# Performance work log

Measured on AMD Instinct MI355X. Metric: run time of the kernel, lower is better.

## Reference

```python
import jax, jax.numpy as jnp
import numpy as np

V = 16384  # points per mesh


def _nn_idx(q, r):
    """1-NN index into r for each row of q. q: [Vq,3], r: [Vr,3] -> [Vq] int32.

    Squared euclidean distance via ||q||^2 - 2 q.r + ||r||^2 (K=1 knn_points).
    """
    d = (jnp.sum(q * q, axis=-1, keepdims=True)
         - 2.0 * (q @ r.T)
         + jnp.sum(r * r, axis=-1)[None, :])  # [Vq, Vr]
    return jnp.argmin(d, axis=1)


def setup_inputs() -> dict:
    key = jax.random.key(0)
    k1, k2, k3, k4 = jax.random.split(key, 4)
    return {
        "pred_vertices": jax.random.normal(k1, (1, V, 3), dtype=jnp.float32),
        "trg_vertices": jax.random.normal(k2, (1, V, 3), dtype=jnp.float32),
        "pred_e": jax.random.normal(k3, (1, V, 3), dtype=jnp.float32),
        "trg_e": jax.random.normal(k4, (1, V, 3), dtype=jnp.float32),
    }


def reference(pred_vertices, trg_vertices, pred_e, trg_e):
    pv = pred_vertices[0]  # [V,3]
    tv = trg_vertices[0]   # [V,3]
    # knn_points runs under torch.no_grad() -> indices are constants
    trg2pred_idx = jax.lax.stop_gradient(_nn_idx(tv, pv))  # [V]
    pred2trg_idx = jax.lax.stop_gradient(_nn_idx(pv, tv))  # [V]
    loss_trg2pred = jnp.mean((trg_e - pred_e[:, trg2pred_idx, :]) ** 2)
    loss_pred2trg = jnp.mean((pred_e - trg_e[:, pred2trg_idx, :]) ** 2)
    return loss_trg2pred + loss_pred2trg
```

## Files before the change

### kernel.cpp

```cpp
#include <hip/hip_runtime.h>
#include <hip/hip_bf16.h>

#define NV 16384
#define NT 256
#define NTILES 512
#define RT_CHUNK 64
#define NCHUNK (NTILES / RT_CHUNK)
#define STG 32
#define QT_PER_BLOCK 8
#define NN_BX (NTILES / QT_PER_BLOCK)
#define RES_QPW 4
#define RES_QPB (4 * RES_QPW)
#define RES_BLOCKS (NV / RES_QPB)
#define NPART (2 * RES_BLOCKS)

typedef __attribute__((ext_vector_type(8))) short bf16x8;
typedef __attribute__((ext_vector_type(16))) float f32x16;

__device__ __forceinline__ short bf16bits(float f) {
    __hip_bfloat16 h = __float2bfloat16(f);
    return *reinterpret_cast<short*>(&h);
}
__device__ __forceinline__ float bf16tof(short s) {
    __hip_bfloat16 h = *reinterpret_cast<__hip_bfloat16*>(&s);
    return __bfloat162float(h);
}
__device__ __forceinline__ unsigned sortable(float f) {
    unsigned u = __float_as_uint(f);
    return (u & 0x80000000u) ? ~u : (u | 0x80000000u);
}
__device__ __forceinline__ float min3f(float a, float b, float c) {
    float r;
    asm("v_min3_f32 %0, %1, %2, %3" : "=v"(r) : "v"(a), "v"(b), "v"(c));
    return r;
}
__device__ __forceinline__ float tree16(const f32x16& c) {
    float t0 = min3f(c[0], c[1], c[2]);
    float t1 = min3f(c[3], c[4], c[5]);
    float t2 = min3f(c[6], c[7], c[8]);
    float t3 = min3f(c[9], c[10], c[11]);
    float t4 = min3f(c[12], c[13], c[14]);
    float s0 = min3f(t0, t1, c[15]);
    float s1 = min3f(t2, t3, t4);
    return fminf(s0, s1);
}

__device__ __forceinline__ bf16x8 make_a(float x, float y, float z, int half) {
    short hx = bf16bits(x), hy = bf16bits(y), hz = bf16bits(z);
    short lx = bf16bits(x - bf16tof(hx));
    short ly = bf16bits(y - bf16tof(hy));
    short lz = bf16bits(z - bf16tof(hz));
    float n  = 0.5f * fmaf(z, z, fmaf(y, y, x * x));
    short nh = bf16bits(n);
    short nl = bf16bits(n - bf16tof(nh));
    bf16x8 v;
    v[0] = half ? hz : hx;  v[1] = half ? nh : hy;
    v[2] = half ? nl : hz;  v[3] = half ? (short)0 : lx;
    v[4] = half ? (short)0 : ly;  v[5] = half ? (short)0 : lz;
    v[6] = half ? (short)0 : hx;  v[7] = half ? (short)0 : hy;
    return v;
}
__device__ __forceinline__ bf16x8 make_b(float x, float y, float z, int half) {
    short hx = bf16bits(x), hy = bf16bits(y), hz = bf16bits(z);
    short nhx = bf16bits(-x), nhy = bf16bits(-y), nhz = bf16bits(-z);
    short nlx = bf16bits(bf16tof(hx) - x);
    short nly = bf16bits(bf16tof(hy) - y);
    short nlz = bf16bits(bf16tof(hz) - z);
    const short one = 0x3F80;
    bf16x8 v;
    v[0] = half ? nlz : nhx;  v[1] = half ? one : nhy;
    v[2] = half ? one : nhz;  v[3] = half ? (short)0 : nhx;
    v[4] = half ? (short)0 : nhy;  v[5] = half ? (short)0 : nhz;
    v[6] = half ? (short)0 : nlx;  v[7] = half ? (short)0 : nly;
    return v;
}

__global__ __launch_bounds__(NT) void prep_kernel(
    const float* __restrict__ pred_v, const float* __restrict__ trg_v,
    short* __restrict__ Apack)
{
    int gid = blockIdx.x * NT + threadIdx.x;
    int d   = gid >> 15;
    int rem = gid & 32767;
    int t   = rem >> 6;
    int l   = rem & 63;
    const float* rpts = d ? trg_v : pred_v;
    int p = t * 32 + (l & 31);
    bf16x8 v = make_a(rpts[3 * p + 0], rpts[3 * p + 1], rpts[3 * p + 2], l >> 5);
    *(bf16x8*)(Apack + ((size_t)gid) * 8) = v;
}

__global__ __launch_bounds__(NT, 4) void nn_mfma_kernel(
    const float* __restrict__ pred_v, const float* __restrict__ trg_v,
    const short* __restrict__ Apack, unsigned long long* __restrict__ results)
{
    __shared__ short lds[STG * 512];
    const int tid = threadIdx.x, lane = tid & 63, w = tid >> 6;
    const int dir = blockIdx.z;
    const float* qpts = dir ? pred_v : trg_v;
    const int qt0 = blockIdx.x * QT_PER_BLOCK + w * 2;
    const int rtb = blockIdx.y * RT_CHUNK;
    const int half = lane >> 5;
    const size_t dbase = (size_t)dir * NTILES * 512;

    const int qp0 = qt0 * 32 + (lane & 31);
    bf16x8 b0 = make_b(qpts[3 * qp0 + 0], qpts[3 * qp0 + 1], qpts[3 * qp0 + 2], half);
    bf16x8 b1 = make_b(qpts[3 * (qp0 + 32) + 0], qpts[3 * (qp0 + 32) + 1],
                       qpts[3 * (qp0 + 32) + 2], half);

    float dmin0 = 1e30f, dmin1 = 1e30f;
    int bp0 = 0, bp1 = 0;
    const f32x16 zc = {};

    for (int g = 0; g < RT_CHUNK / STG; g++) {
        __syncthreads();
        const bf16x8* src = (const bf16x8*)(Apack + dbase + (size_t)(rtb + g * STG) * 512);
#pragma unroll
        for (int s = 0; s < (STG * 64) / NT; s++) {
            int slot = s * NT + tid;
            *(bf16x8*)(&lds[slot * 8]) = src[slot];
        }
        __syncthreads();
#pragma unroll 2
        for (int p = 0; p < STG / 2; p++) {
            bf16x8 a0 = *(const bf16x8*)(&lds[(2 * p) * 512 + lane * 8]);
            f32x16 c0 = __builtin_amdgcn_mfma_f32_32x32x16_bf16(a0, b0, zc, 0, 0, 0);
            f32x16 c1 = __builtin_amdgcn_mfma_f32_32x32x16_bf16(a0, b1, zc, 0, 0, 0);
            float u0 = tree16(c0), u1 = tree16(c1);
            bf16x8 a1 = *(const bf16x8*)(&lds[(2 * p + 1) * 512 + lane * 8]);
            f32x16 d0 = __builtin_amdgcn_mfma_f32_32x32x16_bf16(a1, b0, zc, 0, 0, 0);
            f32x16 d1 = __builtin_amdgcn_mfma_f32_32x32x16_bf16(a1, b1, zc, 0, 0, 0);
            float m0 = fminf(u0, tree16(d0));
            float m1 = fminf(u1, tree16(d1));
            int pid = blockIdx.y * (RT_CHUNK / 2) + g * (STG / 2) + p;
            bool lt0 = m0 < dmin0; dmin0 = lt0 ? m0 : dmin0; bp0 = lt0 ? pid : bp0;
            bool lt1 = m1 < dmin1; dmin1 = lt1 ? m1 : dmin1; bp1 = lt1 ? pid : bp1;
        }
    }

    unsigned long long k0 = ((unsigned long long)sortable(dmin0) << 32) | (unsigned)bp0;
    unsigned long long k1 = ((unsigned long long)sortable(dmin1) << 32) | (unsigned)bp1;
    unsigned long long o0 = __shfl_xor(k0, 32); k0 = (o0 < k0) ? o0 : k0;
    unsigned long long o1 = __shfl_xor(k1, 32); k1 = (o1 < k1) ? o1 : k1;
    if (lane < 32) {
        size_t base = ((size_t)dir * NCHUNK + blockIdx.y) * NV;
        results[base + qt0 * 32 + lane] = k0;
        results[base + (qt0 + 1) * 32 + lane] = k1;
    }
}

__global__ __launch_bounds__(NT) void resolve_loss_kernel(
    const float* __restrict__ pred_v, const float* __restrict__ trg_v,
    const float* __restrict__ pred_e, const float* __restrict__ trg_e,
    const unsigned long long* __restrict__ results, float* __restrict__ partials)
{
    const int dir = blockIdx.y;
    const float* qpts = dir ? pred_v : trg_v;
    const float* rpts = dir ? trg_v : pred_v;
    const float* qe_b = dir ? pred_e : trg_e;
    const float* re_b = dir ? trg_e : pred_e;

    const int tid = threadIdx.x, lane = tid & 63, wv = tid >> 6;
    float acc = 0.0f;

    for (int qq = 0; qq < RES_QPW; qq++) {
        const int q = blockIdx.x * RES_QPB + wv * RES_QPW + qq;

        unsigned long long key = 0xFFFFFFFFFFFFFFFFULL;
        if (lane < NCHUNK)
            key = results[((size_t)dir * NCHUNK + lane) * NV + q];
        unsigned long long o;
        o = __shfl_xor(key, 4); key = (o < key) ? o : key;
        o = __shfl_xor(key, 2); key = (o < key) ? o : key;
        o = __shfl_xor(key, 1); key = (o < key) ? o : key;
        key = __shfl(key, 0);
        const int pair = (int)(unsigned)(key & 0xFFFFFFFFULL);
        const int i = pair * 64 + lane;

        float nqx = -qpts[3 * q + 0], nqy = -qpts[3 * q + 1], nqz = -qpts[3 * q + 2];
        float x = rpts[3 * i + 0], y = rpts[3 * i + 1], z = rpts[3 * i + 2];
        float rw = 0.5f * fmaf(z, z, fmaf(y, y, x * x));
        float s = fmaf(nqx, x, rw);
        s = fmaf(nqy, y, s);
        s = fmaf(nqz, z, s);

        unsigned long long kk = ((unsigned long long)sortable(s) << 32) | (unsigned)i;
#pragma unroll
        for (int off = 32; off > 0; off >>= 1) {
            unsigned long long t = __shfl_xor(kk, off);
            kk = (t < kk) ? t : kk;
        }
        if (lane == 0) {
            int j = (int)(unsigned)(kk & 0xFFFFFFFFULL);
            float dx = qe_b[3 * q + 0] - re_b[3 * j + 0];
            float dy = qe_b[3 * q + 1] - re_b[3 * j + 1];
            float dz = qe_b[3 * q + 2] - re_b[3 * j + 2];
            acc += fmaf(dx, dx, fmaf(dy, dy, dz * dz));
        }
    }

    __shared__ float wsum[4];
    if (lane == 0) wsum[wv] = acc;
    __syncthreads();
    if (tid == 0)
        partials[dir * RES_BLOCKS + blockIdx.x] =
            (wsum[0] + wsum[1]) + (wsum[2] + wsum[3]);
}

__global__ __launch_bounds__(NT) void final_kernel(
    const float* __restrict__ partials, float* __restrict__ out)
{
    const int tid = threadIdx.x;
    float acc = 0.0f;
#pragma unroll
    for (int t = 0; t < NPART / NT; t++) acc += partials[t * NT + tid];
    __shared__ float red[NT];
    red[tid] = acc;
    __syncthreads();
    for (int s = NT / 2; s > 0; s >>= 1) {
        if (tid < s) red[tid] += red[tid + s];
        __syncthreads();
    }
    if (tid == 0) out[0] = red[0] * (1.0f / 49152.0f);
}

extern "C" void kernel_launch(void* const* d_in, const int* in_sizes, int n_in,
                              void* d_out, int out_size, void* d_ws, size_t ws_size,
                              hipStream_t stream) {
    const float* pred_v = (const float*)d_in[0];
    const float* trg_v  = (const float*)d_in[1];
    const float* pred_e = (const float*)d_in[2];
    const float* trg_e  = (const float*)d_in[3];
    float* out = (float*)d_out;

    unsigned long long* results = (unsigned long long*)d_ws;
    short* Apack = (short*)(results + 2 * NCHUNK * NV);
    float* partials = (float*)(Apack + 2 * NTILES * 512);

    prep_kernel<<<(2 * NTILES * 64) / NT, NT, 0, stream>>>(pred_v, trg_v, Apack);

    nn_mfma_kernel<<<dim3(NN_BX, NCHUNK, 2), NT, 0, stream>>>(
        pred_v, trg_v, Apack, results);

    resolve_loss_kernel<<<dim3(RES_BLOCKS, 2), NT, 0, stream>>>(
        pred_v, trg_v, pred_e, trg_e, results, partials);

    final_kernel<<<1, NT, 0, stream>>>(partials, out);
}
```

Baseline: 39.48 us.

## Fuse nearest-neighbor MFMA search with exact refinement and loss in one kernel

Merges the chunked MFMA nearest-neighbor kernel and the resolve/loss kernel into one. Each block now owns one 32-query tile and scans all 512 reference tiles, with its four waves splitting the reference range and combining their results through LDS. Wave 0 then refines exactly over the 32 points of the winning tile and reduces the loss contribution. This removes the intermediate results buffer, its global round trip and one launch. The cost is that every block streams the whole packed reference set through LDS, and each A fragment is reused for only one query tile instead of two. That multiplies cache traffic and shrinks the parallel grid per direction.

```diff
diff --git a/kernel.cpp b/kernel.cpp
--- a/kernel.cpp
+++ b/kernel.cpp
@@ -4,15 +4,10 @@
 #define NV 16384
 #define NT 256
 #define NTILES 512
-#define RT_CHUNK 64
-#define NCHUNK (NTILES / RT_CHUNK)
-#define STG 32
-#define QT_PER_BLOCK 8
-#define NN_BX (NTILES / QT_PER_BLOCK)
-#define RES_QPW 4
-#define RES_QPB (4 * RES_QPW)
-#define RES_BLOCKS (NV / RES_QPB)
-#define NPART (2 * RES_BLOCKS)
+#define WPT 128
+#define RPB 8
+#define ROUNDS (WPT / RPB)
+#define NPART (2 * NTILES)
 
 typedef __attribute__((ext_vector_type(8))) short bf16x8;
 typedef __attribute__((ext_vector_type(16))) float f32x16;
@@ -90,130 +85,107 @@
     *(bf16x8*)(Apack + ((size_t)gid) * 8) = v;
 }
 
-__global__ __launch_bounds__(NT, 4) void nn_mfma_kernel(
-    const float* __restrict__ pred_v, const float* __restrict__ trg_v,
-    const short* __restrict__ Apack, unsigned long long* __restrict__ results)
-{
-    __shared__ short lds[STG * 512];
-    const int tid = threadIdx.x, lane = tid & 63, w = tid >> 6;
-    const int dir = blockIdx.z;
-    const float* qpts = dir ? pred_v : trg_v;
-    const int qt0 = blockIdx.x * QT_PER_BLOCK + w * 2;
-    const int rtb = blockIdx.y * RT_CHUNK;
-    const int half = lane >> 5;
-    const size_t dbase = (size_t)dir * NTILES * 512;
-
-    const int qp0 = qt0 * 32 + (lane & 31);
-    bf16x8 b0 = make_b(qpts[3 * qp0 + 0], qpts[3 * qp0 + 1], qpts[3 * qp0 + 2], half);
-    bf16x8 b1 = make_b(qpts[3 * (qp0 + 32) + 0], qpts[3 * (qp0 + 32) + 1],
-                       qpts[3 * (qp0 + 32) + 2], half);
-
-    float dmin0 = 1e30f, dmin1 = 1e30f;
-    int bp0 = 0, bp1 = 0;
-    const f32x16 zc = {};
-
-    for (int g = 0; g < RT_CHUNK / STG; g++) {
-        __syncthreads();
-        const bf16x8* src = (const bf16x8*)(Apack + dbase + (size_t)(rtb + g * STG) * 512);
-#pragma unroll
-        for (int s = 0; s < (STG * 64) / NT; s++) {
-            int slot = s * NT + tid;
-            *(bf16x8*)(&lds[slot * 8]) = src[slot];
-        }
-        __syncthreads();
-#pragma unroll 2
-        for (int p = 0; p < STG / 2; p++) {
-            bf16x8 a0 = *(const bf16x8*)(&lds[(2 * p) * 512 + lane * 8]);
-            f32x16 c0 = __builtin_amdgcn_mfma_f32_32x32x16_bf16(a0, b0, zc, 0, 0, 0);
-            f32x16 c1 = __builtin_amdgcn_mfma_f32_32x32x16_bf16(a0, b1, zc, 0, 0, 0);
-            float u0 = tree16(c0), u1 = tree16(c1);
-            bf16x8 a1 = *(const bf16x8*)(&lds[(2 * p + 1) * 512 + lane * 8]);
-            f32x16 d0 = __builtin_amdgcn_mfma_f32_32x32x16_bf16(a1, b0, zc, 0, 0, 0);
-            f32x16 d1 = __builtin_amdgcn_mfma_f32_32x32x16_bf16(a1, b1, zc, 0, 0, 0);
-            float m0 = fminf(u0, tree16(d0));
-            float m1 = fminf(u1, tree16(d1));
-            int pid = blockIdx.y * (RT_CHUNK / 2) + g * (STG / 2) + p;
-            bool lt0 = m0 < dmin0; dmin0 = lt0 ? m0 : dmin0; bp0 = lt0 ? pid : bp0;
-            bool lt1 = m1 < dmin1; dmin1 = lt1 ? m1 : dmin1; bp1 = lt1 ? pid : bp1;
-        }
-    }
-
-    unsigned long long k0 = ((unsigned long long)sortable(dmin0) << 32) | (unsigned)bp0;
-    unsigned long long k1 = ((unsigned long long)sortable(dmin1) << 32) | (unsigned)bp1;
-    unsigned long long o0 = __shfl_xor(k0, 32); k0 = (o0 < k0) ? o0 : k0;
-    unsigned long long o1 = __shfl_xor(k1, 32); k1 = (o1 < k1) ? o1 : k1;
-    if (lane < 32) {
-        size_t base = ((size_t)dir * NCHUNK + blockIdx.y) * NV;
-        results[base + qt0 * 32 + lane] = k0;
-        results[base + (qt0 + 1) * 32 + lane] = k1;
-    }
-}
-
-__global__ __launch_bounds__(NT) void resolve_loss_kernel(
+__global__ __launch_bounds__(NT) void fused_kernel(
     const float* __restrict__ pred_v, const float* __restrict__ trg_v,
     const float* __restrict__ pred_e, const float* __restrict__ trg_e,
-    const unsigned long long* __restrict__ results, float* __restrict__ partials)
+    const short* __restrict__ Apack, float* __restrict__ partials)
 {
+    __shared__ short lds[32 * 512];
+    const int tid = threadIdx.x, lane = tid & 63, w = tid >> 6;
     const int dir = blockIdx.y;
+    const int qt  = blockIdx.x;
     const float* qpts = dir ? pred_v : trg_v;
     const float* rpts = dir ? trg_v : pred_v;
     const float* qe_b = dir ? pred_e : trg_e;
     const float* re_b = dir ? trg_e : pred_e;
-
-    const int tid = threadIdx.x, lane = tid & 63, wv = tid >> 6;
-    float acc = 0.0f;
-
-    for (int qq = 0; qq < RES_QPW; qq++) {
-        const int q = blockIdx.x * RES_QPB + wv * RES_QPW + qq;
-
-        unsigned long long key = 0xFFFFFFFFFFFFFFFFULL;
-        if (lane < NCHUNK)
-            key = results[((size_t)dir * NCHUNK + lane) * NV + q];
-        unsigned long long o;
-        o = __shfl_xor(key, 4); key = (o < key) ? o : key;
-        o = __shfl_xor(key, 2); key = (o < key) ? o : key;
-        o = __shfl_xor(key, 1); key = (o < key) ? o : key;
-        key = __shfl(key, 0);
-        const int pair = (int)(unsigned)(key & 0xFFFFFFFFULL);
-        const int i = pair * 64 + lane;
-
-        float nqx = -qpts[3 * q + 0], nqy = -qpts[3 * q + 1], nqz = -qpts[3 * q + 2];
-        float x = rpts[3 * i + 0], y = rpts[3 * i + 1], z = rpts[3 * i + 2];
+    const bf16x8* Avec = (const bf16x8*)Apack + (size_t)dir * NTILES * 64;
+    bf16x8* ldsv = (bf16x8*)lds;
+
+    const int half = lane >> 5;
+    const int qp0 = qt * 32 + (lane & 31);
+    const bf16x8 b0 = make_b(qpts[3 * qp0 + 0], qpts[3 * qp0 + 1], qpts[3 * qp0 + 2], half);
+
+    float dmin = 1e30f;
+    int bp = 0;
+    const f32x16 zc = {};
+
+    for (int r = 0; r < ROUNDS; r++) {
+        __syncthreads();
+#pragma unroll
+        for (int it = 0; it < 8; it++) {
+            int g = it * NT + tid;
+            int chunk = g >> 9, within = g & 511;
+            ldsv[g] = Avec[(chunk * WPT + r * RPB) * 64 + within];
+        }
+        __syncthreads();
+#pragma unroll 4
+        for (int i = 0; i < RPB; i++) {
+            bf16x8 a = ldsv[(w * RPB + i) * 64 + lane];
+            int tile = w * WPT + r * RPB + i;
+            f32x16 c = __builtin_amdgcn_mfma_f32_32x32x16_bf16(a, b0, zc, 0, 0, 0);
+            float m = tree16(c);
+            bool lt = m < dmin;
+            dmin = lt ? m : dmin;
+            bp = lt ? tile : bp;
+        }
+    }
+
+    unsigned long long key = ((unsigned long long)sortable(dmin) << 32) | (unsigned)bp;
+    { unsigned long long o = __shfl_xor(key, 32); key = (o < key) ? o : key; }
+
+    __syncthreads();
+    unsigned long long* kl = (unsigned long long*)lds;
+    if (w > 0 && lane < 32) kl[(w - 1) * 32 + lane] = key;
+    __syncthreads();
+    if (w != 0) return;
+
+#pragma unroll
+    for (int j = 0; j < 3; j++) {
+        unsigned long long o = kl[j * 32 + (lane & 31)];
+        key = (o < key) ? o : key;
+    }
+
+    const int tile = (int)(unsigned)(key & 0xFFFFFFFFULL);
+    const float nqx = -qpts[3 * qp0 + 0];
+    const float nqy = -qpts[3 * qp0 + 1];
+    const float nqz = -qpts[3 * qp0 + 2];
+    float dm = 1e30f;
+    int jm = tile * 32;
+    const int p0 = tile * 32 + half * 16;
+#pragma unroll 4
+    for (int pt = 0; pt < 16; pt++) {
+        int j = p0 + pt;
+        float x = rpts[3 * j + 0], y = rpts[3 * j + 1], z = rpts[3 * j + 2];
         float rw = 0.5f * fmaf(z, z, fmaf(y, y, x * x));
         float s = fmaf(nqx, x, rw);
         s = fmaf(nqy, y, s);
         s = fmaf(nqz, z, s);
-
-        unsigned long long kk = ((unsigned long long)sortable(s) << 32) | (unsigned)i;
+        bool lt = s < dm;
+        dm = lt ? s : dm;
+        jm = lt ? j : jm;
+    }
+    unsigned long long kk = ((unsigned long long)sortable(dm) << 32) | (unsigned)jm;
+    { unsigned long long o = __shfl_xor(kk, 32); kk = (o < kk) ? o : kk; }
+
+    float contrib = 0.0f;
+    if (lane < 32) {
+        int j = (int)(unsigned)(kk & 0xFFFFFFFFULL);
+        float dx = qe_b[3 * qp0 + 0] - re_b[3 * j + 0];
+        float dy = qe_b[3 * qp0 + 1] - re_b[3 * j + 1];
+        float dz = qe_b[3 * qp0 + 2] - re_b[3 * j + 2];
+        contrib = fmaf(dx, dx, fmaf(dy, dy, dz * dz));
+    }
 #pragma unroll
-        for (int off = 32; off > 0; off >>= 1) {
-            unsigned long long t = __shfl_xor(kk, off);
-            kk = (t < kk) ? t : kk;
-        }
-        if (lane == 0) {
-            int j = (int)(unsigned)(kk & 0xFFFFFFFFULL);
-            float dx = qe_b[3 * q + 0] - re_b[3 * j + 0];
-            float dy = qe_b[3 * q + 1] - re_b[3 * j + 1];
-            float dz = qe_b[3 * q + 2] - re_b[3 * j + 2];
-            acc += fmaf(dx, dx, fmaf(dy, dy, dz * dz));
-        }
-    }
-
-    __shared__ float wsum[4];
-    if (lane == 0) wsum[wv] = acc;
-    __syncthreads();
-    if (tid == 0)
-        partials[dir * RES_BLOCKS + blockIdx.x] =
-            (wsum[0] + wsum[1]) + (wsum[2] + wsum[3]);
+    for (int off = 32; off > 0; off >>= 1) contrib += __shfl_xor(contrib, off);
+    if (lane == 0) partials[dir * NTILES + qt] = contrib;
 }
 
 __global__ __launch_bounds__(NT) void final_kernel(
     const float* __restrict__ partials, float* __restrict__ out)
 {
     const int tid = threadIdx.x;
-    float acc = 0.0f;
-#pragma unroll
-    for (int t = 0; t < NPART / NT; t++) acc += partials[t * NT + tid];
+    float acc = (partials[tid] + partials[tid + 256])
+              + (partials[tid + 512] + partials[tid + 768]);
     __shared__ float red[NT];
     red[tid] = acc;
     __syncthreads();
@@ -233,17 +205,13 @@
     const float* trg_e  = (const float*)d_in[3];
     float* out = (float*)d_out;
 
-    unsigned long long* results = (unsigned long long*)d_ws;
-    short* Apack = (short*)(results + 2 * NCHUNK * NV);
+    short* Apack = (short*)d_ws;
     float* partials = (float*)(Apack + 2 * NTILES * 512);
 
     prep_kernel<<<(2 * NTILES * 64) / NT, NT, 0, stream>>>(pred_v, trg_v, Apack);
 
-    nn_mfma_kernel<<<dim3(NN_BX, NCHUNK, 2), NT, 0, stream>>>(
-        pred_v, trg_v, Apack, results);
-
-    resolve_loss_kernel<<<dim3(RES_BLOCKS, 2), NT, 0, stream>>>(
-        pred_v, trg_v, pred_e, trg_e, results, partials);
+    fused_kernel<<<dim3(NTILES, 2), NT, 0, stream>>>(
+        pred_v, trg_v, pred_e, trg_e, Apack, partials);
 
     final_kernel<<<1, NT, 0, stream>>>(partials, out);
 }
```

Result: slower. 54.06 us (+36.9%).

## Stream reference tiles directly from global memory instead of LDS staging in NN kernel

Applied to the files above, without the earlier changes.

The nearest-neighbour MFMA kernel no longer stages reference tiles through shared memory with barriers. Each wave now reads its A operand straight from global memory (L2-cached) and tracks the best single 32-point tile rather than a tile pair. The resolve kernel therefore rescans 32 candidates per query instead of 64. MFMA is issued via inline asm, and the occupancy hint in launch_bounds is dropped. The aim is to remove LDS copy and sync overhead, at the risk of exposing global-load latency, and redundant per-wave reads.

```diff
diff --git a/kernel.cpp b/kernel.cpp
--- a/kernel.cpp
+++ b/kernel.cpp
@@ -4,13 +4,12 @@
 #define NV 16384
 #define NT 256
 #define NTILES 512
-#define RT_CHUNK 64
-#define NCHUNK (NTILES / RT_CHUNK)
-#define STG 32
-#define QT_PER_BLOCK 8
-#define NN_BX (NTILES / QT_PER_BLOCK)
+#define NCH 8
+#define CHT (NTILES / NCH)
+#define QPW 2
+#define NN_BX (NTILES / (4 * QPW))
 #define RES_QPW 4
-#define RES_QPB (4 * RES_QPW)
+#define RES_QPB 16
 #define RES_BLOCKS (NV / RES_QPB)
 #define NPART (2 * RES_BLOCKS)
 
@@ -43,6 +42,13 @@
     float s0 = min3f(t0, t1, c[15]);
     float s1 = min3f(t2, t3, t4);
     return fminf(s0, s1);
+}
+
+__device__ __forceinline__ f32x16 mfma_tile(bf16x8 a, bf16x8 b, f32x16 zc) {
+    f32x16 d;
+    asm("v_mfma_f32_32x32x16_bf16 %0, %1, %2, %3"
+        : "=&v"(d) : "v"(a), "v"(b), "v"(zc));
+    return d;
 }
 
 __device__ __forceinline__ bf16x8 make_a(float x, float y, float z, int half) {
@@ -90,60 +96,49 @@
     *(bf16x8*)(Apack + ((size_t)gid) * 8) = v;
 }
 
-__global__ __launch_bounds__(NT, 4) void nn_mfma_kernel(
+__global__ __launch_bounds__(NT) void nn_mfma_kernel(
     const float* __restrict__ pred_v, const float* __restrict__ trg_v,
     const short* __restrict__ Apack, unsigned long long* __restrict__ results)
 {
-    __shared__ short lds[STG * 512];
     const int tid = threadIdx.x, lane = tid & 63, w = tid >> 6;
-    const int dir = blockIdx.z;
+    const int dir = blockIdx.z, ch = blockIdx.y;
     const float* qpts = dir ? pred_v : trg_v;
-    const int qt0 = blockIdx.x * QT_PER_BLOCK + w * 2;
-    const int rtb = blockIdx.y * RT_CHUNK;
+    const int qt0 = (blockIdx.x * 4 + w) * QPW;
     const int half = lane >> 5;
-    const size_t dbase = (size_t)dir * NTILES * 512;
+    const bf16x8* Avec = (const bf16x8*)Apack + (size_t)dir * NTILES * 64;
 
     const int qp0 = qt0 * 32 + (lane & 31);
     bf16x8 b0 = make_b(qpts[3 * qp0 + 0], qpts[3 * qp0 + 1], qpts[3 * qp0 + 2], half);
     bf16x8 b1 = make_b(qpts[3 * (qp0 + 32) + 0], qpts[3 * (qp0 + 32) + 1],
                        qpts[3 * (qp0 + 32) + 2], half);
 
+    f32x16 zc = {};
     float dmin0 = 1e30f, dmin1 = 1e30f;
     int bp0 = 0, bp1 = 0;
-    const f32x16 zc = {};
-
-    for (int g = 0; g < RT_CHUNK / STG; g++) {
-        __syncthreads();
-        const bf16x8* src = (const bf16x8*)(Apack + dbase + (size_t)(rtb + g * STG) * 512);
-#pragma unroll
-        for (int s = 0; s < (STG * 64) / NT; s++) {
-            int slot = s * NT + tid;
-            *(bf16x8*)(&lds[slot * 8]) = src[slot];
-        }
-        __syncthreads();
+
+    const bf16x8* ap = Avec + (size_t)(ch * CHT) * 64 + lane;
 #pragma unroll 2
-        for (int p = 0; p < STG / 2; p++) {
-            bf16x8 a0 = *(const bf16x8*)(&lds[(2 * p) * 512 + lane * 8]);
-            f32x16 c0 = __builtin_amdgcn_mfma_f32_32x32x16_bf16(a0, b0, zc, 0, 0, 0);
-            f32x16 c1 = __builtin_amdgcn_mfma_f32_32x32x16_bf16(a0, b1, zc, 0, 0, 0);
-            float u0 = tree16(c0), u1 = tree16(c1);
-            bf16x8 a1 = *(const bf16x8*)(&lds[(2 * p + 1) * 512 + lane * 8]);
-            f32x16 d0 = __builtin_amdgcn_mfma_f32_32x32x16_bf16(a1, b0, zc, 0, 0, 0);
-            f32x16 d1 = __builtin_amdgcn_mfma_f32_32x32x16_bf16(a1, b1, zc, 0, 0, 0);
-            float m0 = fminf(u0, tree16(d0));
-            float m1 = fminf(u1, tree16(d1));
-            int pid = blockIdx.y * (RT_CHUNK / 2) + g * (STG / 2) + p;
-            bool lt0 = m0 < dmin0; dmin0 = lt0 ? m0 : dmin0; bp0 = lt0 ? pid : bp0;
-            bool lt1 = m1 < dmin1; dmin1 = lt1 ? m1 : dmin1; bp1 = lt1 ? pid : bp1;
-        }
+    for (int t = 0; t < CHT; t++) {
+        bf16x8 a = ap[t * 64];
+        int tile = ch * CHT + t;
+        f32x16 d0 = mfma_tile(a, b0, zc);
+        float m0 = tree16(d0);
+        bool l0 = m0 < dmin0;
+        dmin0 = l0 ? m0 : dmin0;
+        bp0 = l0 ? tile : bp0;
+        f32x16 d1 = mfma_tile(a, b1, zc);
+        float m1 = tree16(d1);
+        bool l1 = m1 < dmin1;
+        dmin1 = l1 ? m1 : dmin1;
+        bp1 = l1 ? tile : bp1;
     }
 
     unsigned long long k0 = ((unsigned long long)sortable(dmin0) << 32) | (unsigned)bp0;
     unsigned long long k1 = ((unsigned long long)sortable(dmin1) << 32) | (unsigned)bp1;
-    unsigned long long o0 = __shfl_xor(k0, 32); k0 = (o0 < k0) ? o0 : k0;
-    unsigned long long o1 = __shfl_xor(k1, 32); k1 = (o1 < k1) ? o1 : k1;
+    { unsigned long long o = __shfl_xor(k0, 32); k0 = (o < k0) ? o : k0; }
+    { unsigned long long o = __shfl_xor(k1, 32); k1 = (o < k1) ? o : k1; }
     if (lane < 32) {
-        size_t base = ((size_t)dir * NCHUNK + blockIdx.y) * NV;
+        size_t base = ((size_t)dir * NCH + ch) * NV;
         results[base + qt0 * 32 + lane] = k0;
         results[base + (qt0 + 1) * 32 + lane] = k1;
     }
@@ -167,15 +162,15 @@
         const int q = blockIdx.x * RES_QPB + wv * RES_QPW + qq;
 
         unsigned long long key = 0xFFFFFFFFFFFFFFFFULL;
-        if (lane < NCHUNK)
-            key = results[((size_t)dir * NCHUNK + lane) * NV + q];
+        if (lane < NCH)
+            key = results[((size_t)dir * NCH + lane) * NV + q];
         unsigned long long o;
         o = __shfl_xor(key, 4); key = (o < key) ? o : key;
         o = __shfl_xor(key, 2); key = (o < key) ? o : key;
         o = __shfl_xor(key, 1); key = (o < key) ? o : key;
         key = __shfl(key, 0);
-        const int pair = (int)(unsigned)(key & 0xFFFFFFFFULL);
-        const int i = pair * 64 + lane;
+        const int tile = (int)(unsigned)(key & 0xFFFFFFFFULL);
+        const int i = tile * 32 + (lane & 31);
 
         float nqx = -qpts[3 * q + 0], nqy = -qpts[3 * q + 1], nqz = -qpts[3 * q + 2];
         float x = rpts[3 * i + 0], y = rpts[3 * i + 1], z = rpts[3 * i + 2];
@@ -234,12 +229,12 @@
     float* out = (float*)d_out;
 
     unsigned long long* results = (unsigned long long*)d_ws;
-    short* Apack = (short*)(results + 2 * NCHUNK * NV);
+    short* Apack = (short*)(results + 2 * NCH * NV);
     float* partials = (float*)(Apack + 2 * NTILES * 512);
 
     prep_kernel<<<(2 * NTILES * 64) / NT, NT, 0, stream>>>(pred_v, trg_v, Apack);
 
-    nn_mfma_kernel<<<dim3(NN_BX, NCHUNK, 2), NT, 0, stream>>>(
+    nn_mfma_kernel<<<dim3(NN_BX, NCH, 2), NT, 0, stream>>>(
         pred_v, trg_v, Apack, results);
 
     resolve_loss_kernel<<<dim3(RES_BLOCKS, 2), NT, 0, stream>>>(
```

Result: slower. 45.84 us (+16.1%).
